# Performance work log

Hardware: AMD Instinct MI355X
Metric: run time of the kernel (lower is better)

The kernel has to match this reference:

```python
import jax, jax.numpy as jnp
import numpy as np
import math

EPS = 1e-5

def _ln(x):
    # LayerNorm over last dim, no affine (elementwise_affine=False)
    m = jnp.mean(x, axis=-1, keepdims=True)
    v = jnp.var(x, axis=-1, keepdims=True)
    return (x - m) / jnp.sqrt(v + EPS)

def setup_inputs() -> dict:
    key = jax.random.key(0)
    ks = jax.random.split(key, 12)
    bs, P, L, D, H, V = 32, 256, 32, 128, 128, 300
    std = 1.0 / math.sqrt(H)
    xav = math.sqrt(2.0 / ((V + 1) + D))
    emb = jax.random.normal(ks[2], (V + 1, D), jnp.float32) * xav
    emb = emb.at[V].set(0.0)  # padding_idx row
    u = lambda k, shp: jax.random.uniform(k, shp, jnp.float32, -std, std)
    return {
        "paths": jax.random.randint(ks[0], (bs, P, L), 0, V + 1),
        "paths_mask": jax.random.randint(ks[1], (bs, P), 1, L + 1),
        "emb": emb,
        "Wi": u(ks[3], (2 * H, D)), "bi": u(ks[4], (2 * H,)),
        "Wh": u(ks[5], (2 * H, H)), "bh": u(ks[6], (2 * H,)),
        "Ww": u(ks[7], (H, D)), "bw": u(ks[8], (H,)),
        "Wu": u(ks[9], (H, H)), "bu": u(ks[10], (H,)),
        "gamma": jnp.ones((2 * H,), jnp.float32),
        "beta": jnp.zeros((2 * H,), jnp.float32),
    }

def reference(paths, paths_mask, emb, Wi, bi, Wh, bh, Ww, bw, Wu, bu, gamma, beta):
    bs, P, L = paths.shape
    D = emb.shape[1]
    H = Ww.shape[0]
    B = bs * P
    # Embed and flatten paths: [L, B, D] (time-major for scan)
    x = emb[paths].reshape(B * L and (B, L, D))  # [B, L, D]
    x = jnp.transpose(x, (1, 0, 2))              # [L, B, D]
    # Input-dependent parts precomputed across all timesteps
    xi = _ln(jnp.einsum('lbd,gd->lbg', x, Wi) + bi)  # [L, B, 2H]
    xw = _ln(jnp.einsum('lbd,hd->lbh', x, Ww) + bw)  # [L, B, H]

    def step(h, xs_t):
        i2h_t, xw_t = xs_t
        h2h = _ln(h @ Wh.T + bh)
        gates = jax.nn.sigmoid(i2h_t + h2h)
        z = gates[:, :H]
        r = gates[:, H:]
        hu = _ln(h @ Wu.T + bu)
        h_hat = jnp.tanh(xw_t + r * hu)
        h_new = (1.0 - z) * h + z * h_hat
        return h_new, h_new

    h0 = jnp.zeros((B, H), x.dtype)
    _, ys = jax.lax.scan(step, h0, (xi, xw))      # ys: [L, B, H]
    lengths = paths_mask.reshape(-1)              # [B]
    out = ys[lengths - 1, jnp.arange(B)]          # [B, H] hidden at last valid step
    out = out.reshape(bs, P, H)
    # interleave forward/backward halves (relation-path pairing)
    fwd = jnp.concatenate([out[:, 0::2, :], out[:, 1::2, :]], axis=-1)
    bwd = jnp.concatenate([out[:, 1::2, :], out[:, 0::2, :]], axis=-1)
    res = jnp.zeros((bs, P, 2 * H), out.dtype)
    res = res.at[:, 0::2, :].set(fwd).at[:, 1::2, :].set(bwd)
    # final affine LayerNorm (gru_ln)
    m = jnp.mean(res, axis=-1, keepdims=True)
    v = jnp.var(res, axis=-1, keepdims=True)
    return (res - m) / jnp.sqrt(v + EPS) * gamma + beta
```

## Files before the change

### kernel.cpp

```cpp
#include <hip/hip_runtime.h>

typedef float  f32x4 __attribute__((ext_vector_type(4)));
typedef short  s16x8 __attribute__((ext_vector_type(8)));

#define LDS_BARRIER() asm volatile("s_waitcnt lgkmcnt(0)\ns_barrier" ::: "memory")

__device__ __forceinline__ unsigned short bfb(float x) {
  unsigned u = __builtin_bit_cast(unsigned, x);
  return (unsigned short)((u + 0x7FFFu + ((u >> 16) & 1u)) >> 16);
}
__device__ __forceinline__ float fast_sig(float x) {
  float e = __builtin_amdgcn_exp2f(x * -1.44269504f);
  return __builtin_amdgcn_rcpf(1.f + e);
}
__device__ __forceinline__ float fast_tanh(float x) {
  float e = __builtin_amdgcn_exp2f(x * 2.88539008f);
  return 1.f - 2.f * __builtin_amdgcn_rcpf(1.f + e);
}

__global__ __launch_bounds__(256) void tab_kernel(
    const float* __restrict__ emb,
    const float* __restrict__ Wi, const float* __restrict__ bi,
    const float* __restrict__ Ww, const float* __restrict__ bw,
    const float* __restrict__ Wh, const float* __restrict__ Wu,
    const int* __restrict__ pmask, int* __restrict__ perm,
    float* __restrict__ xi_tab, float* __restrict__ xw_tab,
    s16x8* __restrict__ frags)
{
  if (blockIdx.x == 309) {
    __shared__ int hist[33];
    __shared__ int base2[33];
    const int tid = threadIdx.x;
    if (tid < 33) hist[tid] = 0;
    __syncthreads();
    for (int i = tid; i < 8192; i += 256) atomicAdd(&hist[pmask[i]], 1);
    __syncthreads();
    if (tid == 0) {
      int acc = 0;
      for (int l = 1; l <= 32; ++l) { base2[l] = acc; acc += hist[l]; }
    }
    __syncthreads();
    for (int i = tid; i < 8192; i += 256) {
      const int pos = atomicAdd(&base2[pmask[i]], 1);
      perm[pos] = i;
    }
    return;
  }
  if (blockIdx.x >= 301) {
    const int T = blockIdx.x - 301;
    const int lane = threadIdx.x;
    if (lane >= 64) return;
    const int a = lane & 15, s = lane >> 4;
    const float* rowp[3];
    rowp[0] = Wh + (16 * T + a) * 128;
    rowp[1] = Wh + (128 + 16 * T + a) * 128;
    rowp[2] = Wu + (16 * T + a) * 128;
    #pragma unroll
    for (int mat = 0; mat < 3; ++mat) {
      #pragma unroll
      for (int kk = 0; kk < 4; ++kk) {
        const float* src = rowp[mat] + 32 * kk + 8 * s;
        const float4 A = *(const float4*)src;
        const float4 B = *(const float4*)(src + 4);
        s16x8 v;
        v[0] = (short)bfb(A.x); v[1] = (short)bfb(A.y);
        v[2] = (short)bfb(A.z); v[3] = (short)bfb(A.w);
        v[4] = (short)bfb(B.x); v[5] = (short)bfb(B.y);
        v[6] = (short)bfb(B.z); v[7] = (short)bfb(B.w);
        frags[((mat * 8 + T) * 4 + kk) * 64 + lane] = v;
      }
    }
    return;
  }

  const int v = blockIdx.x;
  const int g = threadIdx.x;
  const float4* er = (const float4*)(emb + v * 128);

  float acc = bi[g];
  const float4* wr = (const float4*)(Wi + g * 128);
  #pragma unroll 8
  for (int j = 0; j < 32; ++j) {
    float4 e = er[j], w4 = wr[j];
    acc = fmaf(e.x, w4.x, acc); acc = fmaf(e.y, w4.y, acc);
    acc = fmaf(e.z, w4.z, acc); acc = fmaf(e.w, w4.w, acc);
  }
  float accw = 0.f;
  if (g < 128) {
    accw = bw[g];
    const float4* wr2 = (const float4*)(Ww + g * 128);
    #pragma unroll 8
    for (int j = 0; j < 32; ++j) {
      float4 e = er[j], w4 = wr2[j];
      accw = fmaf(e.x, w4.x, accw); accw = fmaf(e.y, w4.y, accw);
      accw = fmaf(e.z, w4.z, accw); accw = fmaf(e.w, w4.w, accw);
    }
  }
  __shared__ float rs[4][2], rw[2][2];
  float s = acc, q = acc * acc;
  #pragma unroll
  for (int m = 1; m < 64; m <<= 1) { s += __shfl_xor(s, m); q += __shfl_xor(q, m); }
  if ((threadIdx.x & 63) == 0) { rs[threadIdx.x >> 6][0] = s; rs[threadIdx.x >> 6][1] = q; }
  float sw_ = accw, qw_ = accw * accw;
  #pragma unroll
  for (int m = 1; m < 64; m <<= 1) { sw_ += __shfl_xor(sw_, m); qw_ += __shfl_xor(qw_, m); }
  if (g < 128 && (g & 63) == 0) { rw[g >> 6][0] = sw_; rw[g >> 6][1] = qw_; }
  __syncthreads();
  const float SH = rs[0][0] + rs[1][0] + rs[2][0] + rs[3][0];
  const float QH = rs[0][1] + rs[1][1] + rs[2][1] + rs[3][1];
  const float mH = SH * (1.f / 256.f);
  const float rH = rsqrtf(fmaxf(QH * (1.f / 256.f) - mH * mH, 0.f) + 1e-5f);
  xi_tab[v * 256 + g] = (acc - mH) * rH;
  if (g < 128) {
    const float SW = rw[0][0] + rw[1][0], QW = rw[0][1] + rw[1][1];
    const float mW = SW * (1.f / 128.f);
    const float rW = rsqrtf(fmaxf(QW * (1.f / 128.f) - mW * mW, 0.f) + 1e-5f);
    xw_tab[v * 128 + g] = (accw - mW) * rW;
  }
}

__global__ __launch_bounds__(256, 2) void rec_kernel(
    const int* __restrict__ paths, const int* __restrict__ pmask,
    const int* __restrict__ perm,
    const float* __restrict__ bh, const float* __restrict__ bu,
    const float* __restrict__ xi_tab, const float* __restrict__ xw_tab,
    const s16x8* __restrict__ frags,
    float* __restrict__ out)
{
  __shared__ unsigned char hbuf[4096];
  __shared__ alignas(16) float red[4][4][16][4];
  __shared__ int plT[512];

  const int tid  = threadIdx.x;
  const int w    = tid >> 6;
  const int lane = tid & 63;
  const int s    = lane >> 4;
  const int r    = lane & 15;
  const int grp  = (blockIdx.x < 256) ? blockIdx.x : 767 - blockIdx.x;
  const int base = grp * 16;
  const int gb0  = 32 * w + 4 * s;

  s16x8 wz[2][4], wr2[2][4], wu2[2][4];
  #pragma unroll
  for (int u = 0; u < 2; ++u) {
    const int T = 2 * w + u;
    #pragma unroll
    for (int kk = 0; kk < 4; ++kk) {
      wz[u][kk]  = frags[((0 * 8 + T) * 4 + kk) * 64 + lane];
      wr2[u][kk] = frags[((1 * 8 + T) * 4 + kk) * 64 + lane];
      wu2[u][kk] = frags[((2 * 8 + T) * 4 + kk) * 64 + lane];
    }
  }
  for (int k = tid; k < 512; k += 256)
    plT[(k >> 4) * 16 + (k & 15)] = paths[perm[base + (k & 15)] * 32 + (k >> 4)];
  ((uint4*)hbuf)[tid] = uint4{0u, 0u, 0u, 0u};

  const int ri  = perm[base + r];
  const int len = pmask[ri];
  const int len_max = __shfl(len, 15);

  f32x4 bz[2], br2[2], bu2[2];
  #pragma unroll
  for (int u = 0; u < 2; ++u) {
    bz[u]  = *(const f32x4*)(bh + gb0 + 16 * u);
    br2[u] = *(const f32x4*)(bh + 128 + gb0 + 16 * u);
    bu2[u] = *(const f32x4*)(bu + gb0 + 16 * u);
  }
  int hoff[4];
  #pragma unroll
  for (int kk = 0; kk < 4; ++kk)
    hoff[kk] = r * 256 + (((4 * kk + s) ^ r) << 4);
  int hwadr[2];
  #pragma unroll
  for (int u = 0; u < 2; ++u)
    hwadr[u] = r * 256 + (((4 * w + 2 * u + (s >> 1)) ^ r) << 4) + (s & 1) * 8;

  f32x4 hold[2] = {f32x4{0.f,0.f,0.f,0.f}, f32x4{0.f,0.f,0.f,0.f}};
  float* orow = out + (size_t)ri * 256 + gb0;

  __syncthreads();

  f32x4 xiz[2], xir[2], xwv[2];
  {
    const int p = plT[r];
    #pragma unroll
    for (int u = 0; u < 2; ++u) {
      xiz[u] = *(const f32x4*)(xi_tab + p * 256 + gb0 + 16 * u);
      xir[u] = *(const f32x4*)(xi_tab + p * 256 + 128 + gb0 + 16 * u);
      xwv[u] = *(const f32x4*)(xw_tab + p * 128 + gb0 + 16 * u);
    }
  }

  #pragma unroll 1
  for (int t = 0; t < len_max; ++t) {
    const int tn = (t + 1 < len_max) ? t + 1 : t;
    const int pn = plT[tn * 16 + r];
    f32x4 nxiz[2], nxir[2], nxwv[2];
    #pragma unroll
    for (int u = 0; u < 2; ++u) {
      nxiz[u] = *(const f32x4*)(xi_tab + pn * 256 + gb0 + 16 * u);
      nxir[u] = *(const f32x4*)(xi_tab + pn * 256 + 128 + gb0 + 16 * u);
      nxwv[u] = *(const f32x4*)(xw_tab + pn * 128 + gb0 + 16 * u);
    }

    f32x4 az[2] = {}, ar[2] = {}, au[2] = {};
    #pragma unroll
    for (int kk = 0; kk < 4; ++kk) {
      const s16x8 hb = *(const s16x8*)(hbuf + hoff[kk]);
      #pragma unroll
      for (int u = 0; u < 2; ++u) {
        az[u] = __builtin_amdgcn_mfma_f32_16x16x32_bf16(wz[u][kk],  hb, az[u], 0, 0, 0);
        ar[u] = __builtin_amdgcn_mfma_f32_16x16x32_bf16(wr2[u][kk], hb, ar[u], 0, 0, 0);
        au[u] = __builtin_amdgcn_mfma_f32_16x16x32_bf16(wu2[u][kk], hb, au[u], 0, 0, 0);
      }
    }

    float sH = 0.f, qH = 0.f, sU = 0.f, qU = 0.f;
    #pragma unroll
    for (int u = 0; u < 2; ++u) {
      #pragma unroll
      for (int i = 0; i < 4; ++i) {
        az[u][i] += bz[u][i];  sH += az[u][i]; qH = fmaf(az[u][i], az[u][i], qH);
        ar[u][i] += br2[u][i]; sH += ar[u][i]; qH = fmaf(ar[u][i], ar[u][i], qH);
        au[u][i] += bu2[u][i]; sU += au[u][i]; qU = fmaf(au[u][i], au[u][i], qU);
      }
    }
    *(f32x4*)&red[w][s][r][0] = f32x4{sH, qH, sU, qU};

    LDS_BARRIER();

    f32x4 acc0 = *(const f32x4*)&red[0][0][r][0];
    f32x4 acc1 = *(const f32x4*)&red[0][1][r][0];
    #pragma unroll
    for (int c = 2; c < 16; c += 2) {
      acc0 += *(const f32x4*)&red[c >> 2][c & 3][r][0];
      acc1 += *(const f32x4*)&red[(c + 1) >> 2][(c + 1) & 3][r][0];
    }
    const f32x4 S = acc0 + acc1;
    const float mH = S[0] * (1.f / 256.f);
    const float rsH = rsqrtf(fmaxf(S[1] * (1.f / 256.f) - mH * mH, 0.f) + 1e-5f);
    const float cH = -mH * rsH;
    const float mU = S[2] * (1.f / 128.f);
    const float rsU = rsqrtf(fmaxf(S[3] * (1.f / 128.f) - mU * mU, 0.f) + 1e-5f);
    const float cU = -mU * rsU;

    f32x4 hn[2];
    #pragma unroll
    for (int u = 0; u < 2; ++u) {
      #pragma unroll
      for (int i = 0; i < 4; ++i) {
        const float zg = fast_sig(xiz[u][i] + fmaf(az[u][i], rsH, cH));
        const float rg = fast_sig(xir[u][i] + fmaf(ar[u][i], rsH, cH));
        const float hu = fmaf(au[u][i], rsU, cU);
        const float hh = fast_tanh(fmaf(rg, hu, xwv[u][i]));
        hn[u][i] = fmaf(zg, hh - hold[u][i], hold[u][i]);
      }
    }
    if (t == len - 1) {
      #pragma unroll
      for (int u = 0; u < 2; ++u)
        *(float4*)(orow + 16 * u) = float4{hn[u][0], hn[u][1], hn[u][2], hn[u][3]};
    }
    #pragma unroll
    for (int u = 0; u < 2; ++u) {
      const unsigned lo  = (unsigned)bfb(hn[u][0]) | ((unsigned)bfb(hn[u][1]) << 16);
      const unsigned hi2 = (unsigned)bfb(hn[u][2]) | ((unsigned)bfb(hn[u][3]) << 16);
      *(uint2*)(hbuf + hwadr[u]) = uint2{lo, hi2};
      hold[u] = hn[u];
      xiz[u] = nxiz[u]; xir[u] = nxir[u]; xwv[u] = nxwv[u];
    }
    LDS_BARRIER();
  }
}

__global__ __launch_bounds__(256) void out_kernel(
    const float* __restrict__ gamma, const float* __restrict__ beta,
    float* __restrict__ out)
{
  const int tid = threadIdx.x;
  const int lane = tid & 63;
  const int m = blockIdx.x * 4 + (tid >> 6);
  float* pa = out + (size_t)(2 * m) * 256;
  float* pb = pa + 256;
  const float oa0 = pa[lane], oa1 = pa[64 + lane];
  const float ob0 = pb[lane], ob1 = pb[64 + lane];
  float s = oa0 + oa1 + ob0 + ob1;
  float q = oa0 * oa0 + oa1 * oa1 + ob0 * ob0 + ob1 * ob1;
  #pragma unroll
  for (int msk = 1; msk < 64; msk <<= 1) { s += __shfl_xor(s, msk); q += __shfl_xor(q, msk); }
  const float mean = s * (1.f / 256.f);
  const float rstd = rsqrtf(fmaxf(q * (1.f / 256.f) - mean * mean, 0.f) + 1e-5f);
  const float g0 = gamma[lane], g1 = gamma[64 + lane], g2 = gamma[128 + lane], g3 = gamma[192 + lane];
  const float b0 = beta[lane],  b1 = beta[64 + lane],  b2 = beta[128 + lane],  b3 = beta[192 + lane];
  const float na0 = (oa0 - mean) * rstd, na1 = (oa1 - mean) * rstd;
  const float nb0 = (ob0 - mean) * rstd, nb1 = (ob1 - mean) * rstd;
  pa[lane]       = na0 * g0 + b0;
  pa[64 + lane]  = na1 * g1 + b1;
  pa[128 + lane] = nb0 * g2 + b2;
  pa[192 + lane] = nb1 * g3 + b3;
  pb[lane]       = nb0 * g0 + b0;
  pb[64 + lane]  = nb1 * g1 + b1;
  pb[128 + lane] = na0 * g2 + b2;
  pb[192 + lane] = na1 * g3 + b3;
}

extern "C" void kernel_launch(void* const* d_in, const int* in_sizes, int n_in,
                              void* d_out, int out_size, void* d_ws, size_t ws_size,
                              hipStream_t stream) {
  const int*   paths = (const int*)d_in[0];
  const int*   pmask = (const int*)d_in[1];
  const float* emb   = (const float*)d_in[2];
  const float* Wi    = (const float*)d_in[3];
  const float* bi    = (const float*)d_in[4];
  const float* Wh    = (const float*)d_in[5];
  const float* bh    = (const float*)d_in[6];
  const float* Ww    = (const float*)d_in[7];
  const float* bw    = (const float*)d_in[8];
  const float* Wu    = (const float*)d_in[9];
  const float* bu    = (const float*)d_in[10];
  const float* gamma = (const float*)d_in[11];
  const float* beta  = (const float*)d_in[12];
  float* out = (float*)d_out;

  float* xi_tab = (float*)d_ws;
  float* xw_tab = xi_tab + 301 * 256;
  s16x8* frags  = (s16x8*)((char*)d_ws + 462336);
  int*   perm   = (int*)((char*)d_ws + 560640);

  hipLaunchKernelGGL(tab_kernel, dim3(310), dim3(256), 0, stream,
                     emb, Wi, bi, Ww, bw, Wh, Wu, pmask, perm, xi_tab, xw_tab, frags);
  hipLaunchKernelGGL(rec_kernel, dim3(512), dim3(256), 0, stream,
                     paths, pmask, perm, bh, bu, xi_tab, xw_tab, frags, out);
  hipLaunchKernelGGL(out_kernel, dim3(1024), dim3(256), 0, stream, gamma, beta, out);
}
```

Before: 75.42 us.

## Interleave two independent row groups per block to overlap MFMA with gate math

```diff
diff --git a/kernel.cpp b/kernel.cpp
--- a/kernel.cpp
+++ b/kernel.cpp
@@ -119,7 +119,97 @@
   }
 }
 
-__global__ __launch_bounds__(256, 2) void rec_kernel(
+
+#define READ_HB(hbv, hbufg)                                                       \
+  _Pragma("unroll")                                                               \
+  for (int kk = 0; kk < 4; ++kk) hbv[kk] = *(const s16x8*)((hbufg) + hoff[kk]);
+
+#define FANIN_LOAD(rv, redg)                                                      \
+  _Pragma("unroll")                                                               \
+  for (int c = 0; c < 16; ++c)                                                    \
+    rv[c] = *(const f32x4*)&(redg)[((c >> 2) * 4 + (c & 3)) * 64 + r * 4];
+
+#define MFMA24(az_, ar_, au_, hbv)                                                \
+  _Pragma("unroll")                                                               \
+  for (int u = 0; u < 2; ++u) {                                                   \
+    az_[u] = f32x4{0.f,0.f,0.f,0.f}; ar_[u] = az_[u]; au_[u] = az_[u];            \
+  }                                                                               \
+  _Pragma("unroll")                                                               \
+  for (int kk = 0; kk < 4; ++kk) {                                                \
+    _Pragma("unroll")                                                             \
+    for (int u = 0; u < 2; ++u) {                                                 \
+      az_[u] = __builtin_amdgcn_mfma_f32_16x16x32_bf16(wz[u][kk],  hbv[kk], az_[u], 0, 0, 0); \
+      ar_[u] = __builtin_amdgcn_mfma_f32_16x16x32_bf16(wr2[u][kk], hbv[kk], ar_[u], 0, 0, 0); \
+      au_[u] = __builtin_amdgcn_mfma_f32_16x16x32_bf16(wu2[u][kk], hbv[kk], au_[u], 0, 0, 0); \
+    }                                                                             \
+  }
+
+#define STATS_G(az_, ar_, au_, redg)                                              \
+  {                                                                               \
+    float s0 = 0.f, s1 = 0.f, q0 = 0.f, q1 = 0.f, su0 = 0.f, qu0 = 0.f;           \
+    _Pragma("unroll")                                                             \
+    for (int u = 0; u < 2; ++u) {                                                 \
+      _Pragma("unroll")                                                           \
+      for (int i = 0; i < 4; ++i) {                                               \
+        az_[u][i] += bz[u][i];  ar_[u][i] += br2[u][i]; au_[u][i] += bu2[u][i];   \
+        if (u == 0) { s0 += az_[u][i]; q0 = fmaf(az_[u][i], az_[u][i], q0);       \
+                      s1 += ar_[u][i]; q1 = fmaf(ar_[u][i], ar_[u][i], q1); }     \
+        else        { s0 += az_[u][i]; q0 = fmaf(az_[u][i], az_[u][i], q0);       \
+                      s1 += ar_[u][i]; q1 = fmaf(ar_[u][i], ar_[u][i], q1); }     \
+        su0 += au_[u][i]; qu0 = fmaf(au_[u][i], au_[u][i], qu0);                  \
+      }                                                                           \
+    }                                                                             \
+    *(f32x4*)&(redg)[(w * 4 + s) * 64 + r * 4] = f32x4{s0 + s1, q0 + q1, su0, qu0}; \
+  }
+
+#define FINISH_G(az_, ar_, au_, rv, xiz_, xir_, xwv_, hold_, hbufg, orow_, len_, lmax_, plTg, t_) \
+  {                                                                               \
+    f32x4 a0 = rv[0] + rv[1], a1 = rv[2] + rv[3];                                 \
+    f32x4 a2 = rv[4] + rv[5], a3 = rv[6] + rv[7];                                 \
+    f32x4 a4 = rv[8] + rv[9], a5 = rv[10] + rv[11];                               \
+    f32x4 a6 = rv[12] + rv[13], a7 = rv[14] + rv[15];                             \
+    const f32x4 S = ((a0 + a1) + (a2 + a3)) + ((a4 + a5) + (a6 + a7));            \
+    const float mH = S[0] * (1.f / 256.f);                                        \
+    const float rsH = rsqrtf(fmaxf(S[1] * (1.f / 256.f) - mH * mH, 0.f) + 1e-5f); \
+    const float cH = -mH * rsH;                                                   \
+    const float mU = S[2] * (1.f / 128.f);                                        \
+    const float rsU = rsqrtf(fmaxf(S[3] * (1.f / 128.f) - mU * mU, 0.f) + 1e-5f); \
+    const float cU = -mU * rsU;                                                   \
+    f32x4 hn[2];                                                                  \
+    _Pragma("unroll")                                                             \
+    for (int u = 0; u < 2; ++u) {                                                 \
+      _Pragma("unroll")                                                           \
+      for (int i = 0; i < 4; ++i) {                                               \
+        const float zg = fast_sig(xiz_[u][i] + fmaf(az_[u][i], rsH, cH));         \
+        const float rg = fast_sig(xir_[u][i] + fmaf(ar_[u][i], rsH, cH));         \
+        const float hu = fmaf(au_[u][i], rsU, cU);                                \
+        const float hh = fast_tanh(fmaf(rg, hu, xwv_[u][i]));                     \
+        hn[u][i] = fmaf(zg, hh - hold_[u][i], hold_[u][i]);                       \
+      }                                                                           \
+    }                                                                             \
+    if ((t_) == (len_) - 1) {                                                     \
+      _Pragma("unroll")                                                           \
+      for (int u = 0; u < 2; ++u)                                                 \
+        *(float4*)((orow_) + 16 * u) = float4{hn[u][0], hn[u][1], hn[u][2], hn[u][3]}; \
+    }                                                                             \
+    _Pragma("unroll")                                                             \
+    for (int u = 0; u < 2; ++u) {                                                 \
+      const unsigned lo  = (unsigned)bfb(hn[u][0]) | ((unsigned)bfb(hn[u][1]) << 16); \
+      const unsigned hi2 = (unsigned)bfb(hn[u][2]) | ((unsigned)bfb(hn[u][3]) << 16); \
+      *(uint2*)((hbufg) + hwadr[u]) = uint2{lo, hi2};                             \
+      hold_[u] = hn[u];                                                           \
+    }                                                                             \
+    const int tn_ = ((t_) + 1 < (lmax_)) ? (t_) + 1 : (t_);                       \
+    const int pn_ = (plTg)[tn_ * 16 + r];                                         \
+    _Pragma("unroll")                                                             \
+    for (int u = 0; u < 2; ++u) {                                                 \
+      xiz_[u] = *(const f32x4*)(xi_tab + pn_ * 256 + gb0 + 16 * u);               \
+      xir_[u] = *(const f32x4*)(xi_tab + pn_ * 256 + 128 + gb0 + 16 * u);         \
+      xwv_[u] = *(const f32x4*)(xw_tab + pn_ * 128 + gb0 + 16 * u);               \
+    }                                                                             \
+  }
+
+__global__ __launch_bounds__(256, 1) void rec_kernel(
     const int* __restrict__ paths, const int* __restrict__ pmask,
     const int* __restrict__ perm,
     const float* __restrict__ bh, const float* __restrict__ bu,
@@ -127,17 +217,16 @@
     const s16x8* __restrict__ frags,
     float* __restrict__ out)
 {
-  __shared__ unsigned char hbuf[4096];
-  __shared__ alignas(16) float red[4][4][16][4];
-  __shared__ int plT[512];
+  __shared__ alignas(16) unsigned char hbuf[2][4096];
+  __shared__ alignas(16) float red[2][1024];
+  __shared__ int plT[2][512];
 
   const int tid  = threadIdx.x;
   const int w    = tid >> 6;
   const int lane = tid & 63;
   const int s    = lane >> 4;
   const int r    = lane & 15;
-  const int grp  = (blockIdx.x < 256) ? blockIdx.x : 767 - blockIdx.x;
-  const int base = grp * 16;
+  const int base = blockIdx.x * 32;
   const int gb0  = 32 * w + 4 * s;
 
   s16x8 wz[2][4], wr2[2][4], wu2[2][4];
@@ -151,13 +240,18 @@
       wu2[u][kk] = frags[((2 * 8 + T) * 4 + kk) * 64 + lane];
     }
   }
-  for (int k = tid; k < 512; k += 256)
-    plT[(k >> 4) * 16 + (k & 15)] = paths[perm[base + (k & 15)] * 32 + (k >> 4)];
+  for (int k = tid; k < 1024; k += 256)
+    plT[k >> 9][((k >> 4) & 31) * 16 + (k & 15)] =
+        paths[perm[base + 16 * (k >> 9) + (k & 15)] * 32 + ((k >> 4) & 31)];
   ((uint4*)hbuf)[tid] = uint4{0u, 0u, 0u, 0u};
-
-  const int ri  = perm[base + r];
-  const int len = pmask[ri];
-  const int len_max = __shfl(len, 15);
+  ((uint4*)hbuf)[256 + tid] = uint4{0u, 0u, 0u, 0u};
+
+  const int riA  = perm[base + r];
+  const int riB  = perm[base + 16 + r];
+  const int lenA = pmask[riA];
+  const int lenB = pmask[riB];
+  const int lenA_max = __shfl(lenA, 15);
+  const int lenB_max = __shfl(lenB, 15);
 
   f32x4 bz[2], br2[2], bu2[2];
   #pragma unroll
@@ -175,99 +269,61 @@
   for (int u = 0; u < 2; ++u)
     hwadr[u] = r * 256 + (((4 * w + 2 * u + (s >> 1)) ^ r) << 4) + (s & 1) * 8;
 
-  f32x4 hold[2] = {f32x4{0.f,0.f,0.f,0.f}, f32x4{0.f,0.f,0.f,0.f}};
-  float* orow = out + (size_t)ri * 256 + gb0;
+  f32x4 holdA[2] = {f32x4{0.f,0.f,0.f,0.f}, f32x4{0.f,0.f,0.f,0.f}};
+  f32x4 holdB[2] = {f32x4{0.f,0.f,0.f,0.f}, f32x4{0.f,0.f,0.f,0.f}};
+  float* orowA = out + (size_t)riA * 256 + gb0;
+  float* orowB = out + (size_t)riB * 256 + gb0;
+
+  f32x4 azA[2], arA[2], auA[2], azB[2], arB[2], auB[2];
+  f32x4 xizA[2], xirA[2], xwvA[2], xizB[2], xirB[2], xwvB[2];
 
   __syncthreads();
 
-  f32x4 xiz[2], xir[2], xwv[2];
   {
-    const int p = plT[r];
+    const int pA = plT[0][r], pB = plT[1][r];
     #pragma unroll
     for (int u = 0; u < 2; ++u) {
-      xiz[u] = *(const f32x4*)(xi_tab + p * 256 + gb0 + 16 * u);
-      xir[u] = *(const f32x4*)(xi_tab + p * 256 + 128 + gb0 + 16 * u);
-      xwv[u] = *(const f32x4*)(xw_tab + p * 128 + gb0 + 16 * u);
-    }
-  }
+      xizA[u] = *(const f32x4*)(xi_tab + pA * 256 + gb0 + 16 * u);
+      xirA[u] = *(const f32x4*)(xi_tab + pA * 256 + 128 + gb0 + 16 * u);
+      xwvA[u] = *(const f32x4*)(xw_tab + pA * 128 + gb0 + 16 * u);
+      xizB[u] = *(const f32x4*)(xi_tab + pB * 256 + gb0 + 16 * u);
+      xirB[u] = *(const f32x4*)(xi_tab + pB * 256 + 128 + gb0 + 16 * u);
+      xwvB[u] = *(const f32x4*)(xw_tab + pB * 128 + gb0 + 16 * u);
+    }
+  }
+  {
+    s16x8 hbv[4];
+    READ_HB(hbv, hbuf[0]);
+    MFMA24(azA, arA, auA, hbv);
+    STATS_G(azA, arA, auA, red[0]);
+  }
+  LDS_BARRIER();
 
   #pragma unroll 1
-  for (int t = 0; t < len_max; ++t) {
-    const int tn = (t + 1 < len_max) ? t + 1 : t;
-    const int pn = plT[tn * 16 + r];
-    f32x4 nxiz[2], nxir[2], nxwv[2];
-    #pragma unroll
-    for (int u = 0; u < 2; ++u) {
-      nxiz[u] = *(const f32x4*)(xi_tab + pn * 256 + gb0 + 16 * u);
-      nxir[u] = *(const f32x4*)(xi_tab + pn * 256 + 128 + gb0 + 16 * u);
-      nxwv[u] = *(const f32x4*)(xw_tab + pn * 128 + gb0 + 16 * u);
-    }
-
-    f32x4 az[2] = {}, ar[2] = {}, au[2] = {};
-    #pragma unroll
-    for (int kk = 0; kk < 4; ++kk) {
-      const s16x8 hb = *(const s16x8*)(hbuf + hoff[kk]);
-      #pragma unroll
-      for (int u = 0; u < 2; ++u) {
-        az[u] = __builtin_amdgcn_mfma_f32_16x16x32_bf16(wz[u][kk],  hb, az[u], 0, 0, 0);
-        ar[u] = __builtin_amdgcn_mfma_f32_16x16x32_bf16(wr2[u][kk], hb, ar[u], 0, 0, 0);
-        au[u] = __builtin_amdgcn_mfma_f32_16x16x32_bf16(wu2[u][kk], hb, au[u], 0, 0, 0);
-      }
-    }
-
-    float sH = 0.f, qH = 0.f, sU = 0.f, qU = 0.f;
-    #pragma unroll
-    for (int u = 0; u < 2; ++u) {
-      #pragma unroll
-      for (int i = 0; i < 4; ++i) {
-        az[u][i] += bz[u][i];  sH += az[u][i]; qH = fmaf(az[u][i], az[u][i], qH);
-        ar[u][i] += br2[u][i]; sH += ar[u][i]; qH = fmaf(ar[u][i], ar[u][i], qH);
-        au[u][i] += bu2[u][i]; sU += au[u][i]; qU = fmaf(au[u][i], au[u][i], qU);
-      }
-    }
-    *(f32x4*)&red[w][s][r][0] = f32x4{sH, qH, sU, qU};
-
+  for (int t = 0; t < lenB_max; ++t) {
+    const bool doA  = (t < lenA_max);
+    const bool doA2 = (t + 1 < lenA_max);
+    {
+      s16x8 hbv[4];
+      READ_HB(hbv, hbuf[1]);
+      f32x4 rv[16];
+      if (doA) FANIN_LOAD(rv, red[0]);
+      MFMA24(azB, arB, auB, hbv);
+      if (doA)
+        FINISH_G(azA, arA, auA, rv, xizA, xirA, xwvA, holdA, hbuf[0],
+                 orowA, lenA, lenA_max, plT[0], t);
+      STATS_G(azB, arB, auB, red[1]);
+    }
     LDS_BARRIER();
-
-    f32x4 acc0 = *(const f32x4*)&red[0][0][r][0];
-    f32x4 acc1 = *(const f32x4*)&red[0][1][r][0];
-    #pragma unroll
-    for (int c = 2; c < 16; c += 2) {
-      acc0 += *(const f32x4*)&red[c >> 2][c & 3][r][0];
-      acc1 += *(const f32x4*)&red[(c + 1) >> 2][(c + 1) & 3][r][0];
-    }
-    const f32x4 S = acc0 + acc1;
-    const float mH = S[0] * (1.f / 256.f);
-    const float rsH = rsqrtf(fmaxf(S[1] * (1.f / 256.f) - mH * mH, 0.f) + 1e-5f);
-    const float cH = -mH * rsH;
-    const float mU = S[2] * (1.f / 128.f);
-    const float rsU = rsqrtf(fmaxf(S[3] * (1.f / 128.f) - mU * mU, 0.f) + 1e-5f);
-    const float cU = -mU * rsU;
-
-    f32x4 hn[2];
-    #pragma unroll
-    for (int u = 0; u < 2; ++u) {
-      #pragma unroll
-      for (int i = 0; i < 4; ++i) {
-        const float zg = fast_sig(xiz[u][i] + fmaf(az[u][i], rsH, cH));
-        const float rg = fast_sig(xir[u][i] + fmaf(ar[u][i], rsH, cH));
-        const float hu = fmaf(au[u][i], rsU, cU);
-        const float hh = fast_tanh(fmaf(rg, hu, xwv[u][i]));
-        hn[u][i] = fmaf(zg, hh - hold[u][i], hold[u][i]);
-      }
-    }
-    if (t == len - 1) {
-      #pragma unroll
-      for (int u = 0; u < 2; ++u)
-        *(float4*)(orow + 16 * u) = float4{hn[u][0], hn[u][1], hn[u][2], hn[u][3]};
-    }
-    #pragma unroll
-    for (int u = 0; u < 2; ++u) {
-      const unsigned lo  = (unsigned)bfb(hn[u][0]) | ((unsigned)bfb(hn[u][1]) << 16);
-      const unsigned hi2 = (unsigned)bfb(hn[u][2]) | ((unsigned)bfb(hn[u][3]) << 16);
-      *(uint2*)(hbuf + hwadr[u]) = uint2{lo, hi2};
-      hold[u] = hn[u];
-      xiz[u] = nxiz[u]; xir[u] = nxir[u]; xwv[u] = nxwv[u];
+    {
+      s16x8 hbv[4];
+      if (doA2) READ_HB(hbv, hbuf[0]);
+      f32x4 rv[16];
+      FANIN_LOAD(rv, red[1]);
+      if (doA2) MFMA24(azA, arA, auA, hbv);
+      FINISH_G(azB, arB, auB, rv, xizB, xirB, xwvB, holdB, hbuf[1],
+               orowB, lenB, lenB_max, plT[1], t);
+      if (doA2) STATS_G(azA, arA, auA, red[0]);
     }
     LDS_BARRIER();
   }
@@ -329,7 +385,7 @@
 
   hipLaunchKernelGGL(tab_kernel, dim3(310), dim3(256), 0, stream,
                      emb, Wi, bi, Ww, bw, Wh, Wu, pmask, perm, xi_tab, xw_tab, frags);
-  hipLaunchKernelGGL(rec_kernel, dim3(512), dim3(256), 0, stream,
+  hipLaunchKernelGGL(rec_kernel, dim3(256), dim3(256), 0, stream,
                      paths, pmask, perm, bh, bu, xi_tab, xw_tab, frags, out);
   hipLaunchKernelGGL(out_kernel, dim3(1024), dim3(256), 0, stream, gamma, beta, out);
 }
```

Result: slower. 124.4 us (+64.9%).

## Fuse final pair LayerNorm into recurrence kernel via per-pair atomic completion flags

Applied to the files above, without the earlier changes.

```diff
diff --git a/kernel.cpp b/kernel.cpp
--- a/kernel.cpp
+++ b/kernel.cpp
@@ -25,7 +25,7 @@
     const float* __restrict__ Wh, const float* __restrict__ Wu,
     const int* __restrict__ pmask, int* __restrict__ perm,
     float* __restrict__ xi_tab, float* __restrict__ xw_tab,
-    s16x8* __restrict__ frags)
+    s16x8* __restrict__ frags, int* __restrict__ pairflag)
 {
   if (blockIdx.x == 309) {
     __shared__ int hist[33];
@@ -44,6 +44,7 @@
       const int pos = atomicAdd(&base2[pmask[i]], 1);
       perm[pos] = i;
     }
+    for (int i = tid; i < 4096; i += 256) pairflag[i] = 0;
     return;
   }
   if (blockIdx.x >= 301) {
@@ -125,6 +126,8 @@
     const float* __restrict__ bh, const float* __restrict__ bu,
     const float* __restrict__ xi_tab, const float* __restrict__ xw_tab,
     const s16x8* __restrict__ frags,
+    const float* __restrict__ gamma, const float* __restrict__ beta,
+    int* __restrict__ pairflag,
     float* __restrict__ out)
 {
   __shared__ unsigned char hbuf[4096];
@@ -203,7 +206,9 @@
       nxwv[u] = *(const f32x4*)(xw_tab + pn * 128 + gb0 + 16 * u);
     }
 
-    f32x4 az[2] = {}, ar[2] = {}, au[2] = {};
+    f32x4 az[2], ar[2], au[2];
+    #pragma unroll
+    for (int u = 0; u < 2; ++u) { az[u] = bz[u]; ar[u] = br2[u]; au[u] = bu2[u]; }
     #pragma unroll
     for (int kk = 0; kk < 4; ++kk) {
       const s16x8 hb = *(const s16x8*)(hbuf + hoff[kk]);
@@ -220,9 +225,9 @@
     for (int u = 0; u < 2; ++u) {
       #pragma unroll
       for (int i = 0; i < 4; ++i) {
-        az[u][i] += bz[u][i];  sH += az[u][i]; qH = fmaf(az[u][i], az[u][i], qH);
-        ar[u][i] += br2[u][i]; sH += ar[u][i]; qH = fmaf(ar[u][i], ar[u][i], qH);
-        au[u][i] += bu2[u][i]; sU += au[u][i]; qU = fmaf(au[u][i], au[u][i], qU);
+        sH += az[u][i]; qH = fmaf(az[u][i], az[u][i], qH);
+        sH += ar[u][i]; qH = fmaf(ar[u][i], ar[u][i], qH);
+        sU += au[u][i]; qU = fmaf(au[u][i], au[u][i], qU);
       }
     }
     *(f32x4*)&red[w][s][r][0] = f32x4{sH, qH, sU, qU};
@@ -271,37 +276,43 @@
     }
     LDS_BARRIER();
   }
-}
-
-__global__ __launch_bounds__(256) void out_kernel(
-    const float* __restrict__ gamma, const float* __restrict__ beta,
-    float* __restrict__ out)
-{
-  const int tid = threadIdx.x;
-  const int lane = tid & 63;
-  const int m = blockIdx.x * 4 + (tid >> 6);
-  float* pa = out + (size_t)(2 * m) * 256;
-  float* pb = pa + 256;
-  const float oa0 = pa[lane], oa1 = pa[64 + lane];
-  const float ob0 = pb[lane], ob1 = pb[64 + lane];
-  float s = oa0 + oa1 + ob0 + ob1;
-  float q = oa0 * oa0 + oa1 * oa1 + ob0 * ob0 + ob1 * ob1;
-  #pragma unroll
-  for (int msk = 1; msk < 64; msk <<= 1) { s += __shfl_xor(s, msk); q += __shfl_xor(q, msk); }
-  const float mean = s * (1.f / 256.f);
-  const float rstd = rsqrtf(fmaxf(q * (1.f / 256.f) - mean * mean, 0.f) + 1e-5f);
+
+  __syncthreads();
+  __threadfence();
   const float g0 = gamma[lane], g1 = gamma[64 + lane], g2 = gamma[128 + lane], g3 = gamma[192 + lane];
   const float b0 = beta[lane],  b1 = beta[64 + lane],  b2 = beta[128 + lane],  b3 = beta[192 + lane];
-  const float na0 = (oa0 - mean) * rstd, na1 = (oa1 - mean) * rstd;
-  const float nb0 = (ob0 - mean) * rstd, nb1 = (ob1 - mean) * rstd;
-  pa[lane]       = na0 * g0 + b0;
-  pa[64 + lane]  = na1 * g1 + b1;
-  pa[128 + lane] = nb0 * g2 + b2;
-  pa[192 + lane] = nb1 * g3 + b3;
-  pb[lane]       = nb0 * g0 + b0;
-  pb[64 + lane]  = nb1 * g1 + b1;
-  pb[128 + lane] = na0 * g2 + b2;
-  pb[192 + lane] = na1 * g3 + b3;
+  #pragma unroll 1
+  for (int k = 0; k < 4; ++k) {
+    const int row = w * 4 + k;
+    const int rid = perm[base + row];
+    const int pair = rid >> 1;
+    int old = 0;
+    if (lane == 0) old = atomicAdd(&pairflag[pair], 1);
+    old = __shfl(old, 0);
+    if (old == 1) {
+      __threadfence();
+      float* pa = out + (size_t)(2 * pair) * 256;
+      float* pb = pa + 256;
+      const float oa0 = pa[lane], oa1 = pa[64 + lane];
+      const float ob0 = pb[lane], ob1 = pb[64 + lane];
+      float ss = oa0 + oa1 + ob0 + ob1;
+      float qq = oa0 * oa0 + oa1 * oa1 + ob0 * ob0 + ob1 * ob1;
+      #pragma unroll
+      for (int msk = 1; msk < 64; msk <<= 1) { ss += __shfl_xor(ss, msk); qq += __shfl_xor(qq, msk); }
+      const float mean = ss * (1.f / 256.f);
+      const float rstd = rsqrtf(fmaxf(qq * (1.f / 256.f) - mean * mean, 0.f) + 1e-5f);
+      const float na0 = (oa0 - mean) * rstd, na1 = (oa1 - mean) * rstd;
+      const float nb0 = (ob0 - mean) * rstd, nb1 = (ob1 - mean) * rstd;
+      pa[lane]       = na0 * g0 + b0;
+      pa[64 + lane]  = na1 * g1 + b1;
+      pa[128 + lane] = nb0 * g2 + b2;
+      pa[192 + lane] = nb1 * g3 + b3;
+      pb[lane]       = nb0 * g0 + b0;
+      pb[64 + lane]  = nb1 * g1 + b1;
+      pb[128 + lane] = na0 * g2 + b2;
+      pb[192 + lane] = na1 * g3 + b3;
+    }
+  }
 }
 
 extern "C" void kernel_launch(void* const* d_in, const int* in_sizes, int n_in,
@@ -322,14 +333,16 @@
   const float* beta  = (const float*)d_in[12];
   float* out = (float*)d_out;
 
-  float* xi_tab = (float*)d_ws;
-  float* xw_tab = xi_tab + 301 * 256;
-  s16x8* frags  = (s16x8*)((char*)d_ws + 462336);
-  int*   perm   = (int*)((char*)d_ws + 560640);
+  float* xi_tab   = (float*)d_ws;
+  float* xw_tab   = xi_tab + 301 * 256;
+  s16x8* frags    = (s16x8*)((char*)d_ws + 462336);
+  int*   perm     = (int*)((char*)d_ws + 560640);
+  int*   pairflag = (int*)((char*)d_ws + 593408);
 
   hipLaunchKernelGGL(tab_kernel, dim3(310), dim3(256), 0, stream,
-                     emb, Wi, bi, Ww, bw, Wh, Wu, pmask, perm, xi_tab, xw_tab, frags);
+                     emb, Wi, bi, Ww, bw, Wh, Wu, pmask, perm, xi_tab, xw_tab,
+                     frags, pairflag);
   hipLaunchKernelGGL(rec_kernel, dim3(512), dim3(256), 0, stream,
-                     paths, pmask, perm, bh, bu, xi_tab, xw_tab, frags, out);
-  hipLaunchKernelGGL(out_kernel, dim3(1024), dim3(256), 0, stream, gamma, beta, out);
-}
+                     paths, pmask, perm, bh, bu, xi_tab, xw_tab, frags,
+                     gamma, beta, pairflag, out);
+}
```

Result: slower. 193.7 us (+156.9%).
